# Kernel optimization log

Measured on AMD Instinct MI355X. Metric: run time of the kernel, lower is better.

Reference implementation:

```python
import jax, jax.numpy as jnp
import numpy as np

B, N, A, H, MID = 256, 128, 15, 32, 256  # batch, nodes(=in_channels), actions, EQL-proxy hidden, critic mid_weight


def _glorot(k, shape):
    lim = float(np.sqrt(6.0 / (shape[0] + shape[1])))
    return jax.random.uniform(k, shape, jnp.float32, -lim, lim)


def setup_inputs() -> dict:
    key = jax.random.key(0)
    ks = jax.random.split(key, 10)
    obs = jax.random.normal(ks[0], (B, N), jnp.float32)
    return dict(
        obs=obs,
        # messenger EQL proxy: 4 -> H -> 1
        mw1=_glorot(ks[1], (4, H)), mb1=jnp.zeros((H,), jnp.float32),
        mw2=_glorot(ks[2], (H, 1)), mb2=jnp.zeros((1,), jnp.float32),
        # actor EQL proxy: 3 -> H -> 1
        aw1=_glorot(ks[3], (3, H)), ab1=jnp.zeros((H,), jnp.float32),
        aw2=_glorot(ks[4], (H, 1)), ab2=jnp.zeros((1,), jnp.float32),
        # critic MLP: N -> MID -> MID -> MID -> 1 (depth=4)
        cw1=_glorot(ks[5], (N, MID)), cb1=jnp.zeros((MID,), jnp.float32),
        cw2=_glorot(ks[6], (MID, MID)), cb2=jnp.zeros((MID,), jnp.float32),
        cw3=_glorot(ks[7], (MID, MID)), cb3=jnp.zeros((MID,), jnp.float32),
        cw4=_glorot(ks[8], (MID, 1)), cb4=jnp.zeros((1,), jnp.float32),
    )


def reference(obs, mw1, mb1, mw2, mb2, aw1, ab1, aw2, ab2,
              cw1, cb1, cw2, cb2, cw3, cb3, cw4, cb4):
    b, n = obs.shape
    coor = jnp.arange(n, dtype=jnp.float32) / n  # append_index coordinate channel
    x = jnp.stack([obs, jnp.broadcast_to(coor, obs.shape)], axis=-1)  # [B,n,2]

    # all-pairs message pass: msg_in[b,i,j] = concat(x[b,i], x[b,j])  -> [B,n,n,4]
    xi = jnp.broadcast_to(x[:, :, None, :], (b, n, n, 2))
    xj = jnp.broadcast_to(x[:, None, :, :], (b, n, n, 2))
    msg_in = jnp.concatenate([xi, xj], axis=-1)
    messages = jax.nn.relu(msg_in @ mw1 + mb1) @ mw2 + mb2  # [B,n,n,1]
    msg = jnp.sum(messages, axis=-2)[..., 0]  # sum over j, squeeze -> [B,n]

    # append_index again on the aggregated messages
    m = jnp.stack([msg, jnp.broadcast_to(coor, msg.shape)], axis=-1)  # [B,n,2]

    # node x action cross: am[b,i,a] = concat(m[b,i], a)  -> [B,n,A,3]
    acts = jnp.arange(A, dtype=jnp.float32)[None, None, :, None]
    mi = jnp.broadcast_to(m[:, :, None, :], (b, n, A, 2))
    aj = jnp.broadcast_to(acts, (b, n, A, 1))
    am = jnp.concatenate([mi, aj], axis=-1)
    am_messages = jax.nn.relu(am @ aw1 + ab1) @ aw2 + ab2  # [B,n,A,1]
    logits = jnp.sum(am_messages, axis=-3)[..., 0]  # sum over nodes (obs_dim=-3) -> [B,A]

    # critic MLP on raw obs
    h = jax.nn.relu(obs @ cw1 + cb1)
    h = jax.nn.relu(h @ cw2 + cb2)
    h = jax.nn.relu(h @ cw3 + cb3)
    value = h @ cw4 + cb4  # [B,1]
    return logits, value
```

## Files before the change

kernel.cpp:

```cpp
#include <hip/hip_runtime.h>

#define BB    256
#define NN    128
#define AA    15
#define HH    32
#define MIDD  256
#define NCRIT 16

typedef _Float16 h2_t  __attribute__((ext_vector_type(2)));
typedef _Float16 f16x8 __attribute__((ext_vector_type(8)));
typedef float    f32x4 __attribute__((ext_vector_type(4)));

struct MsgS {
    _Float16 vh[NN][HH];
    float4   p4[8][NN];
    float    part[4][16][8];
    float    msg[NN];
};
struct CriS {
    _Float16 hA[2][16][264];
};

__global__ __launch_bounds__(512, 4) void gacq_v9(
    const float* __restrict__ obs,
    const float* __restrict__ mw1, const float* __restrict__ mb1,
    const float* __restrict__ mw2, const float* __restrict__ mb2,
    const float* __restrict__ aw1, const float* __restrict__ ab1,
    const float* __restrict__ aw2, const float* __restrict__ ab2,
    const float* __restrict__ cw1, const float* __restrict__ cb1,
    const float* __restrict__ cw2, const float* __restrict__ cb2,
    const float* __restrict__ cw3, const float* __restrict__ cb3,
    const float* __restrict__ cw4, const float* __restrict__ cb4,
    float* __restrict__ out)
{
    __shared__ __align__(16) float aux_s[356];
    __shared__ __align__(16) float obs_s[NN];
    __shared__ __align__(16) union { MsgS m; CriS c; } u_s;

    const int blk  = blockIdx.x;
    const int t    = threadIdx.x;
    const int lane = t & 63;

    if (blk >= NCRIT) {
        const int b = blk - NCRIT;

        if (t < 354) {
            float v;
            if      (t < 128) v = mw1[t];
            else if (t < 224) v = aw1[t - 128];
            else if (t < 256) v = ab1[t - 224];
            else if (t < 288) v = aw2[t - 256];
            else if (t < 320) v = mw2[t - 288];
            else if (t < 352) v = mb1[t - 320];
            else if (t == 352) v = mb2[0];
            else               v = ab2[0];
            aux_s[t] = v;
        }
        if (t < NN) obs_s[t] = obs[b * NN + t];
        __syncthreads();

        for (int e = t; e < NN * HH / 2; e += 512) {
            const int   j  = e >> 4, kp = e & 15;
            const int   k0 = kp * 2;
            const float cj = (float)j * (1.0f / (float)NN);
            const float v0 = obs_s[j] * aux_s[64 + k0]     + cj * aux_s[96 + k0]     + aux_s[320 + k0];
            const float v1 = obs_s[j] * aux_s[64 + k0 + 1] + cj * aux_s[96 + k0 + 1] + aux_s[320 + k0 + 1];
            h2_t p; p[0] = (_Float16)v0; p[1] = (_Float16)v1;
            *(h2_t*)&u_s.m.vh[j][k0] = p;
        }

        const int kg = t & 7;
        const int rg = (t >> 3) & 15;
        const int jg = t >> 7;

        h2_t u2[8][2], w2h[2];
        w2h[0][0] = (_Float16)aux_s[288 + kg * 4 + 0];
        w2h[0][1] = (_Float16)aux_s[288 + kg * 4 + 1];
        w2h[1][0] = (_Float16)aux_s[288 + kg * 4 + 2];
        w2h[1][1] = (_Float16)aux_s[288 + kg * 4 + 3];
#pragma unroll
        for (int rr = 0; rr < 8; ++rr) {
            const int   row = rg * 8 + rr;
            const float ob  = obs_s[row];
            const float cr  = (float)row * (1.0f / (float)NN);
#pragma unroll
            for (int kp = 0; kp < 2; ++kp) {
                const int k0 = kg * 4 + kp * 2;
                u2[rr][kp][0] = (_Float16)(ob * aux_s[k0]     + cr * aux_s[32 + k0]);
                u2[rr][kp][1] = (_Float16)(ob * aux_s[k0 + 1] + cr * aux_s[32 + k0 + 1]);
            }
        }
        __syncthreads();

        float acc[8];
#pragma unroll
        for (int rr = 0; rr < 8; ++rr) acc[rr] = 0.f;
        const int j0 = jg * 32;
        {
            const h2_t   zero  = (h2_t)((_Float16)0);
            const uint2* vbase = (const uint2*)&u_s.m.vh[0][kg * 4];
            uint2 vc = vbase[j0 * 8];
#pragma unroll 4
            for (int jj = 0; jj < 32; ++jj) {
                const int   nj = j0 + ((jj + 1) & 31);
                const uint2 vn = vbase[nj * 8];
                const h2_t  va = __builtin_bit_cast(h2_t, vc.x);
                const h2_t  vb = __builtin_bit_cast(h2_t, vc.y);
#pragma unroll
                for (int rr = 0; rr < 8; ++rr) {
                    h2_t s0 = u2[rr][0] + va;
                    h2_t s1 = u2[rr][1] + vb;
                    s0 = __builtin_elementwise_max(s0, zero);
                    s1 = __builtin_elementwise_max(s1, zero);
                    acc[rr] = __builtin_amdgcn_fdot2(s0, w2h[0], acc[rr], false);
                    acc[rr] = __builtin_amdgcn_fdot2(s1, w2h[1], acc[rr], false);
                }
                vc = vn;
            }
        }
#pragma unroll
        for (int m = 1; m <= 4; m <<= 1)
#pragma unroll
            for (int rr = 0; rr < 8; ++rr) acc[rr] += __shfl_xor(acc[rr], m);
        if (kg == 0) {
            *(float4*)&u_s.m.part[jg][rg][0] = make_float4(acc[0], acc[1], acc[2], acc[3]);
            *(float4*)&u_s.m.part[jg][rg][4] = make_float4(acc[4], acc[5], acc[6], acc[7]);
        }
        __syncthreads();

        if (t < NN) {
            float m = (float)NN * aux_s[352];
#pragma unroll
            for (int g = 0; g < 4; ++g) m += u_s.m.part[g][t >> 3][t & 7];
            u_s.m.msg[t] = m;
        }
        __syncthreads();

#pragma unroll
        for (int it = 0; it < 2; ++it) {
            const int   row = t & 127;
            const int   c   = (t >> 7) + it * 4;
            const float mi  = u_s.m.msg[row];
            const float cr  = (float)row * (1.0f / (float)NN);
            const int   k0  = c * 4;
            float4 p;
            p.x = mi * aux_s[128 + k0 + 0] + cr * aux_s[160 + k0 + 0] + aux_s[224 + k0 + 0];
            p.y = mi * aux_s[128 + k0 + 1] + cr * aux_s[160 + k0 + 1] + aux_s[224 + k0 + 1];
            p.z = mi * aux_s[128 + k0 + 2] + cr * aux_s[160 + k0 + 2] + aux_s[224 + k0 + 2];
            p.w = mi * aux_s[128 + k0 + 3] + cr * aux_s[160 + k0 + 3] + aux_s[224 + k0 + 3];
            u_s.m.p4[c][row] = p;
        }
        __syncthreads();

        {
            const int   a   = t >> 5;
            const int   sub = t & 31;
            const float fa  = (float)a;
            float qa[HH];
#pragma unroll
            for (int k = 0; k < HH; ++k) qa[k] = fa * aux_s[192 + k];
            float s0 = 0.f, s1 = 0.f, s2 = 0.f, s3 = 0.f;
#pragma unroll
            for (int m = 0; m < 4; ++m) {
                const int row = sub + 32 * m;
#pragma unroll
                for (int c = 0; c < 8; ++c) {
                    const float4 p4 = u_s.m.p4[c][row];
                    const float4 w4 = *(const float4*)&aux_s[256 + c * 4];
                    const int    k0 = c * 4;
                    s0 += fmaxf(p4.x + qa[k0 + 0], 0.f) * w4.x;
                    s1 += fmaxf(p4.y + qa[k0 + 1], 0.f) * w4.y;
                    s2 += fmaxf(p4.z + qa[k0 + 2], 0.f) * w4.z;
                    s3 += fmaxf(p4.w + qa[k0 + 3], 0.f) * w4.w;
                }
            }
            float s = (s0 + s1) + (s2 + s3);
#pragma unroll
            for (int off = 1; off < 32; off <<= 1) s += __shfl_xor(s, off);
            if (sub == 0 && a < AA)
                out[b * AA + a] = s + (float)NN * aux_s[353];
        }
    } else {
        const int b0 = blk * 16;

        for (int e = t; e < 16 * NN; e += 512)
            u_s.c.hA[0][e >> 7][e & 127] = (_Float16)obs[(b0 + (e >> 7)) * NN + (e & 127)];
        __syncthreads();

        const int w    = t >> 6;
        const int arow = lane & 15;
        const int koff = (lane >> 4) * 8;
        const int n0   = w * 32;

        auto critLayer = [&](const _Float16 (&Ain)[16][264], _Float16 (&Aout)[16][264],
                             const float* __restrict__ W, const float* __restrict__ bias,
                             const int Kd) {
            f32x4 acc0 = {0.f, 0.f, 0.f, 0.f};
            f32x4 acc1 = {0.f, 0.f, 0.f, 0.f};
            for (int ks = 0; ks < Kd; ks += 32) {
                const f16x8  af = *(const f16x8*)&Ain[arow][ks + koff];
                const float* wp = W + (size_t)(ks + koff) * MIDD + n0 + arow;
                f16x8 bf0, bf1;
#pragma unroll
                for (int j = 0; j < 8; ++j) {
                    bf0[j] = (_Float16)wp[j * MIDD];
                    bf1[j] = (_Float16)wp[j * MIDD + 16];
                }
                acc0 = __builtin_amdgcn_mfma_f32_16x16x32_f16(af, bf0, acc0, 0, 0, 0);
                acc1 = __builtin_amdgcn_mfma_f32_16x16x32_f16(af, bf1, acc1, 0, 0, 0);
            }
            const float b0v = bias[n0 + arow];
            const float b1v = bias[n0 + 16 + arow];
#pragma unroll
            for (int reg = 0; reg < 4; ++reg) {
                const int i = (lane >> 4) * 4 + reg;
                Aout[i][n0 + arow]      = (_Float16)fmaxf(acc0[reg] + b0v, 0.f);
                Aout[i][n0 + 16 + arow] = (_Float16)fmaxf(acc1[reg] + b1v, 0.f);
            }
        };

        critLayer(u_s.c.hA[0], u_s.c.hA[1], cw1, cb1, 128);
        __syncthreads();
        critLayer(u_s.c.hA[1], u_s.c.hA[0], cw2, cb2, 256);
        __syncthreads();
        critLayer(u_s.c.hA[0], u_s.c.hA[1], cw3, cb3, 256);
        __syncthreads();

        {
            const int i  = t >> 5;
            const int sl = t & 31;
            float s = 0.f;
#pragma unroll
            for (int j = 0; j < 8; ++j)
                s += (float)u_s.c.hA[1][i][sl * 8 + j] * cw4[sl * 8 + j];
#pragma unroll
            for (int off = 1; off < 32; off <<= 1) s += __shfl_xor(s, off);
            if (sl == 0) out[BB * AA + b0 + i] = s + cb4[0];
        }
    }
}

extern "C" void kernel_launch(void* const* d_in, const int* in_sizes, int n_in,
                              void* d_out, int out_size, void* d_ws, size_t ws_size,
                              hipStream_t stream) {
    const float* obs = (const float*)d_in[0];
    const float* mw1 = (const float*)d_in[1];
    const float* mb1 = (const float*)d_in[2];
    const float* mw2 = (const float*)d_in[3];
    const float* mb2 = (const float*)d_in[4];
    const float* aw1 = (const float*)d_in[5];
    const float* ab1 = (const float*)d_in[6];
    const float* aw2 = (const float*)d_in[7];
    const float* ab2 = (const float*)d_in[8];
    const float* cw1 = (const float*)d_in[9];
    const float* cb1 = (const float*)d_in[10];
    const float* cw2 = (const float*)d_in[11];
    const float* cb2 = (const float*)d_in[12];
    const float* cw3 = (const float*)d_in[13];
    const float* cb3 = (const float*)d_in[14];
    const float* cw4 = (const float*)d_in[15];
    const float* cb4 = (const float*)d_in[16];
    float* out = (float*)d_out;

    gacq_v9<<<dim3(BB + NCRIT), dim3(512), 0, stream>>>(
        obs, mw1, mb1, mw2, mb2, aw1, ab1, aw2, ab2,
        cw1, cb1, cw2, cb2, cw3, cb3, cw4, cb4, out);
}
```

Measured before the change: 17.16 us.

## Double block size to 1024 threads, halving per-thread work in all phases

Launches 1024 threads per block instead of 512 and re-splits every phase across them. The message loop now covers 16 j-columns per thread group instead of 32, and the 8 partial sums are reduced straight into the actor projection, which removes one barrier and the msg buffer. Each critic wave computes one 16-column MFMA tile instead of two. This buys more latency hiding and shorter per-thread serial chains, at the cost of heavier register pressure under launch_bounds(1024,4), fewer blocks resident per CU, and more redundant weight reads for the critic.

```diff
diff --git a/kernel.cpp b/kernel.cpp
--- a/kernel.cpp
+++ b/kernel.cpp
@@ -14,14 +14,13 @@
 struct MsgS {
     _Float16 vh[NN][HH];
     float4   p4[8][NN];
-    float    part[4][16][8];
-    float    msg[NN];
+    float    part[8][16][8];
 };
 struct CriS {
     _Float16 hA[2][16][264];
 };
 
-__global__ __launch_bounds__(512, 4) void gacq_v9(
+__global__ __launch_bounds__(1024, 4) void gacq_v10(
     const float* __restrict__ obs,
     const float* __restrict__ mw1, const float* __restrict__ mb1,
     const float* __restrict__ mw2, const float* __restrict__ mb2,
@@ -56,10 +55,12 @@
             else               v = ab2[0];
             aux_s[t] = v;
         }
-        if (t < NN) obs_s[t] = obs[b * NN + t];
-        __syncthreads();
-
-        for (int e = t; e < NN * HH / 2; e += 512) {
+        if (t >= 512 && t < 512 + NN) obs_s[t - 512] = obs[b * NN + (t - 512)];
+        __syncthreads();
+
+#pragma unroll
+        for (int it = 0; it < 2; ++it) {
+            const int   e  = t + it * 1024;
             const int   j  = e >> 4, kp = e & 15;
             const int   k0 = kp * 2;
             const float cj = (float)j * (1.0f / (float)NN);
@@ -95,14 +96,14 @@
         float acc[8];
 #pragma unroll
         for (int rr = 0; rr < 8; ++rr) acc[rr] = 0.f;
-        const int j0 = jg * 32;
+        const int j0 = jg * 16;
         {
             const h2_t   zero  = (h2_t)((_Float16)0);
             const uint2* vbase = (const uint2*)&u_s.m.vh[0][kg * 4];
             uint2 vc = vbase[j0 * 8];
 #pragma unroll 4
-            for (int jj = 0; jj < 32; ++jj) {
-                const int   nj = j0 + ((jj + 1) & 31);
+            for (int jj = 0; jj < 16; ++jj) {
+                const int   nj = j0 + ((jj + 1) & 15);
                 const uint2 vn = vbase[nj * 8];
                 const h2_t  va = __builtin_bit_cast(h2_t, vc.x);
                 const h2_t  vb = __builtin_bit_cast(h2_t, vc.y);
@@ -128,21 +129,14 @@
         }
         __syncthreads();
 
-        if (t < NN) {
-            float m = (float)NN * aux_s[352];
-#pragma unroll
-            for (int g = 0; g < 4; ++g) m += u_s.m.part[g][t >> 3][t & 7];
-            u_s.m.msg[t] = m;
-        }
-        __syncthreads();
-
-#pragma unroll
-        for (int it = 0; it < 2; ++it) {
-            const int   row = t & 127;
-            const int   c   = (t >> 7) + it * 4;
-            const float mi  = u_s.m.msg[row];
-            const float cr  = (float)row * (1.0f / (float)NN);
-            const int   k0  = c * 4;
+        {
+            const int row = t & 127;
+            const int c   = t >> 7;
+            float mi = (float)NN * aux_s[352];
+#pragma unroll
+            for (int g = 0; g < 8; ++g) mi += u_s.m.part[g][row >> 3][row & 7];
+            const float cr = (float)row * (1.0f / (float)NN);
+            const int   k0 = c * 4;
             float4 p;
             p.x = mi * aux_s[128 + k0 + 0] + cr * aux_s[160 + k0 + 0] + aux_s[224 + k0 + 0];
             p.y = mi * aux_s[128 + k0 + 1] + cr * aux_s[160 + k0 + 1] + aux_s[224 + k0 + 1];
@@ -153,16 +147,16 @@
         __syncthreads();
 
         {
-            const int   a   = t >> 5;
-            const int   sub = t & 31;
+            const int   a   = t >> 6;
+            const int   sub = lane;
             const float fa  = (float)a;
             float qa[HH];
 #pragma unroll
             for (int k = 0; k < HH; ++k) qa[k] = fa * aux_s[192 + k];
             float s0 = 0.f, s1 = 0.f, s2 = 0.f, s3 = 0.f;
 #pragma unroll
-            for (int m = 0; m < 4; ++m) {
-                const int row = sub + 32 * m;
+            for (int m = 0; m < 2; ++m) {
+                const int row = sub + 64 * m;
 #pragma unroll
                 for (int c = 0; c < 8; ++c) {
                     const float4 p4 = u_s.m.p4[c][row];
@@ -176,46 +170,42 @@
             }
             float s = (s0 + s1) + (s2 + s3);
 #pragma unroll
-            for (int off = 1; off < 32; off <<= 1) s += __shfl_xor(s, off);
+            for (int off = 1; off < 64; off <<= 1) s += __shfl_xor(s, off);
             if (sub == 0 && a < AA)
                 out[b * AA + a] = s + (float)NN * aux_s[353];
         }
     } else {
         const int b0 = blk * 16;
 
-        for (int e = t; e < 16 * NN; e += 512)
+#pragma unroll
+        for (int it = 0; it < 2; ++it) {
+            const int e = t + it * 1024;
             u_s.c.hA[0][e >> 7][e & 127] = (_Float16)obs[(b0 + (e >> 7)) * NN + (e & 127)];
+        }
         __syncthreads();
 
         const int w    = t >> 6;
         const int arow = lane & 15;
         const int koff = (lane >> 4) * 8;
-        const int n0   = w * 32;
+        const int n0   = w * 16;
 
         auto critLayer = [&](const _Float16 (&Ain)[16][264], _Float16 (&Aout)[16][264],
                              const float* __restrict__ W, const float* __restrict__ bias,
                              const int Kd) {
-            f32x4 acc0 = {0.f, 0.f, 0.f, 0.f};
-            f32x4 acc1 = {0.f, 0.f, 0.f, 0.f};
+            f32x4 acc = {0.f, 0.f, 0.f, 0.f};
             for (int ks = 0; ks < Kd; ks += 32) {
                 const f16x8  af = *(const f16x8*)&Ain[arow][ks + koff];
                 const float* wp = W + (size_t)(ks + koff) * MIDD + n0 + arow;
-                f16x8 bf0, bf1;
-#pragma unroll
-                for (int j = 0; j < 8; ++j) {
-                    bf0[j] = (_Float16)wp[j * MIDD];
-                    bf1[j] = (_Float16)wp[j * MIDD + 16];
-                }
-                acc0 = __builtin_amdgcn_mfma_f32_16x16x32_f16(af, bf0, acc0, 0, 0, 0);
-                acc1 = __builtin_amdgcn_mfma_f32_16x16x32_f16(af, bf1, acc1, 0, 0, 0);
-            }
-            const float b0v = bias[n0 + arow];
-            const float b1v = bias[n0 + 16 + arow];
+                f16x8 bf;
+#pragma unroll
+                for (int j = 0; j < 8; ++j) bf[j] = (_Float16)wp[j * MIDD];
+                acc = __builtin_amdgcn_mfma_f32_16x16x32_f16(af, bf, acc, 0, 0, 0);
+            }
+            const float bv = bias[n0 + arow];
 #pragma unroll
             for (int reg = 0; reg < 4; ++reg) {
                 const int i = (lane >> 4) * 4 + reg;
-                Aout[i][n0 + arow]      = (_Float16)fmaxf(acc0[reg] + b0v, 0.f);
-                Aout[i][n0 + 16 + arow] = (_Float16)fmaxf(acc1[reg] + b1v, 0.f);
+                Aout[i][n0 + arow] = (_Float16)fmaxf(acc[reg] + bv, 0.f);
             }
         };
 
@@ -227,15 +217,14 @@
         __syncthreads();
 
         {
-            const int i  = t >> 5;
-            const int sl = t & 31;
+            const int i = t >> 6;
             float s = 0.f;
 #pragma unroll
-            for (int j = 0; j < 8; ++j)
-                s += (float)u_s.c.hA[1][i][sl * 8 + j] * cw4[sl * 8 + j];
-#pragma unroll
-            for (int off = 1; off < 32; off <<= 1) s += __shfl_xor(s, off);
-            if (sl == 0) out[BB * AA + b0 + i] = s + cb4[0];
+            for (int j = 0; j < 4; ++j)
+                s += (float)u_s.c.hA[1][i][lane * 4 + j] * cw4[lane * 4 + j];
+#pragma unroll
+            for (int off = 1; off < 64; off <<= 1) s += __shfl_xor(s, off);
+            if (lane == 0) out[BB * AA + b0 + i] = s + cb4[0];
         }
     }
 }
@@ -262,7 +251,7 @@
     const float* cb4 = (const float*)d_in[16];
     float* out = (float*)d_out;
 
-    gacq_v9<<<dim3(BB + NCRIT), dim3(512), 0, stream>>>(
+    gacq_v10<<<dim3(BB + NCRIT), dim3(1024), 0, stream>>>(
         obs, mw1, mb1, mw2, mb2, aw1, ab1, aw2, ab2,
         cw1, cb1, cw2, cb2, cw3, cb3, cw4, cb4, out);
 }
```

New measurement: 21.96 us. 1.28x slower.

## Keep message-pass operands in registers, one wave per 16-row tile

Applied to the files above, without the earlier changes.

Each wave now owns 16 rows and splits the 128 j columns across 8 lane groups. Every thread computes its own 16 j-side fp16 hidden values in registers, so the shared-memory vh table and its barrier go away. The reduction is done entirely with wave shuffles, which removes the part/msg shared buffers and two __syncthreads. The cost is more register pressure (u2, v2 and acc at 16 each), redundant computation of the j-side values across waves, and a longer shuffle reduction chain.

```diff
diff --git a/kernel.cpp b/kernel.cpp
--- a/kernel.cpp
+++ b/kernel.cpp
@@ -11,17 +11,10 @@
 typedef _Float16 f16x8 __attribute__((ext_vector_type(8)));
 typedef float    f32x4 __attribute__((ext_vector_type(4)));
 
-struct MsgS {
-    _Float16 vh[NN][HH];
-    float4   p4[8][NN];
-    float    part[4][16][8];
-    float    msg[NN];
-};
-struct CriS {
-    _Float16 hA[2][16][264];
-};
-
-__global__ __launch_bounds__(512, 4) void gacq_v9(
+struct MsgS { float4   p4[8][NN]; };
+struct CriS { _Float16 hA[2][16][264]; };
+
+__global__ __launch_bounds__(512, 4) void gacq_v11(
     const float* __restrict__ obs,
     const float* __restrict__ mw1, const float* __restrict__ mb1,
     const float* __restrict__ mw2, const float* __restrict__ mb2,
@@ -40,6 +33,7 @@
     const int blk  = blockIdx.x;
     const int t    = threadIdx.x;
     const int lane = t & 63;
+    const int w    = t >> 6;
 
     if (blk >= NCRIT) {
         const int b = blk - NCRIT;
@@ -59,28 +53,19 @@
         if (t < NN) obs_s[t] = obs[b * NN + t];
         __syncthreads();
 
-        for (int e = t; e < NN * HH / 2; e += 512) {
-            const int   j  = e >> 4, kp = e & 15;
-            const int   k0 = kp * 2;
-            const float cj = (float)j * (1.0f / (float)NN);
-            const float v0 = obs_s[j] * aux_s[64 + k0]     + cj * aux_s[96 + k0]     + aux_s[320 + k0];
-            const float v1 = obs_s[j] * aux_s[64 + k0 + 1] + cj * aux_s[96 + k0 + 1] + aux_s[320 + k0 + 1];
-            h2_t p; p[0] = (_Float16)v0; p[1] = (_Float16)v1;
-            *(h2_t*)&u_s.m.vh[j][k0] = p;
-        }
-
-        const int kg = t & 7;
-        const int rg = (t >> 3) & 15;
-        const int jg = t >> 7;
-
-        h2_t u2[8][2], w2h[2];
+        const int kg = lane & 7;
+        const int jg = (lane >> 3) & 7;
+
+        h2_t w2h[2];
         w2h[0][0] = (_Float16)aux_s[288 + kg * 4 + 0];
         w2h[0][1] = (_Float16)aux_s[288 + kg * 4 + 1];
         w2h[1][0] = (_Float16)aux_s[288 + kg * 4 + 2];
         w2h[1][1] = (_Float16)aux_s[288 + kg * 4 + 3];
-#pragma unroll
-        for (int rr = 0; rr < 8; ++rr) {
-            const int   row = rg * 8 + rr;
+
+        h2_t u2[16][2];
+#pragma unroll
+        for (int rr = 0; rr < 16; ++rr) {
+            const int   row = w * 16 + rr;
             const float ob  = obs_s[row];
             const float cr  = (float)row * (1.0f / (float)NN);
 #pragma unroll
@@ -90,24 +75,31 @@
                 u2[rr][kp][1] = (_Float16)(ob * aux_s[k0 + 1] + cr * aux_s[32 + k0 + 1]);
             }
         }
-        __syncthreads();
-
-        float acc[8];
-#pragma unroll
-        for (int rr = 0; rr < 8; ++rr) acc[rr] = 0.f;
-        const int j0 = jg * 32;
-        {
-            const h2_t   zero  = (h2_t)((_Float16)0);
-            const uint2* vbase = (const uint2*)&u_s.m.vh[0][kg * 4];
-            uint2 vc = vbase[j0 * 8];
-#pragma unroll 4
-            for (int jj = 0; jj < 32; ++jj) {
-                const int   nj = j0 + ((jj + 1) & 31);
-                const uint2 vn = vbase[nj * 8];
-                const h2_t  va = __builtin_bit_cast(h2_t, vc.x);
-                const h2_t  vb = __builtin_bit_cast(h2_t, vc.y);
-#pragma unroll
-                for (int rr = 0; rr < 8; ++rr) {
+        h2_t v2[16][2];
+#pragma unroll
+        for (int jj = 0; jj < 16; ++jj) {
+            const int   j  = jg * 16 + jj;
+            const float ob = obs_s[j];
+            const float cj = (float)j * (1.0f / (float)NN);
+#pragma unroll
+            for (int kp = 0; kp < 2; ++kp) {
+                const int k0 = kg * 4 + kp * 2;
+                v2[jj][kp][0] = (_Float16)(ob * aux_s[64 + k0]     + cj * aux_s[96 + k0]     + aux_s[320 + k0]);
+                v2[jj][kp][1] = (_Float16)(ob * aux_s[64 + k0 + 1] + cj * aux_s[96 + k0 + 1] + aux_s[320 + k0 + 1]);
+            }
+        }
+
+        float acc[16];
+#pragma unroll
+        for (int rr = 0; rr < 16; ++rr) acc[rr] = 0.f;
+        {
+            const h2_t zero = (h2_t)((_Float16)0);
+#pragma unroll
+            for (int jj = 0; jj < 16; ++jj) {
+                const h2_t va = v2[jj][0];
+                const h2_t vb = v2[jj][1];
+#pragma unroll
+                for (int rr = 0; rr < 16; ++rr) {
                     h2_t s0 = u2[rr][0] + va;
                     h2_t s1 = u2[rr][1] + vb;
                     s0 = __builtin_elementwise_max(s0, zero);
@@ -115,40 +107,32 @@
                     acc[rr] = __builtin_amdgcn_fdot2(s0, w2h[0], acc[rr], false);
                     acc[rr] = __builtin_amdgcn_fdot2(s1, w2h[1], acc[rr], false);
                 }
-                vc = vn;
-            }
-        }
-#pragma unroll
-        for (int m = 1; m <= 4; m <<= 1)
-#pragma unroll
-            for (int rr = 0; rr < 8; ++rr) acc[rr] += __shfl_xor(acc[rr], m);
-        if (kg == 0) {
-            *(float4*)&u_s.m.part[jg][rg][0] = make_float4(acc[0], acc[1], acc[2], acc[3]);
-            *(float4*)&u_s.m.part[jg][rg][4] = make_float4(acc[4], acc[5], acc[6], acc[7]);
-        }
-        __syncthreads();
-
-        if (t < NN) {
-            float m = (float)NN * aux_s[352];
-#pragma unroll
-            for (int g = 0; g < 4; ++g) m += u_s.m.part[g][t >> 3][t & 7];
-            u_s.m.msg[t] = m;
-        }
-        __syncthreads();
-
-#pragma unroll
-        for (int it = 0; it < 2; ++it) {
-            const int   row = t & 127;
-            const int   c   = (t >> 7) + it * 4;
-            const float mi  = u_s.m.msg[row];
+            }
+        }
+#pragma unroll
+        for (int m = 1; m <= 32; m <<= 1)
+#pragma unroll
+            for (int rr = 0; rr < 16; ++rr) acc[rr] += __shfl_xor(acc[rr], m);
+
+        {
+            const int rrL = lane & 15;
+            float mi = acc[0];
+#pragma unroll
+            for (int r2 = 1; r2 < 16; ++r2) mi = (rrL == r2) ? acc[r2] : mi;
+            mi += (float)NN * aux_s[352];
+            const int   row = w * 16 + rrL;
             const float cr  = (float)row * (1.0f / (float)NN);
-            const int   k0  = c * 4;
-            float4 p;
-            p.x = mi * aux_s[128 + k0 + 0] + cr * aux_s[160 + k0 + 0] + aux_s[224 + k0 + 0];
-            p.y = mi * aux_s[128 + k0 + 1] + cr * aux_s[160 + k0 + 1] + aux_s[224 + k0 + 1];
-            p.z = mi * aux_s[128 + k0 + 2] + cr * aux_s[160 + k0 + 2] + aux_s[224 + k0 + 2];
-            p.w = mi * aux_s[128 + k0 + 3] + cr * aux_s[160 + k0 + 3] + aux_s[224 + k0 + 3];
-            u_s.m.p4[c][row] = p;
+#pragma unroll
+            for (int cc = 0; cc < 2; ++cc) {
+                const int c  = (lane >> 4) + cc * 4;
+                const int k0 = c * 4;
+                float4 p;
+                p.x = mi * aux_s[128 + k0 + 0] + cr * aux_s[160 + k0 + 0] + aux_s[224 + k0 + 0];
+                p.y = mi * aux_s[128 + k0 + 1] + cr * aux_s[160 + k0 + 1] + aux_s[224 + k0 + 1];
+                p.z = mi * aux_s[128 + k0 + 2] + cr * aux_s[160 + k0 + 2] + aux_s[224 + k0 + 2];
+                p.w = mi * aux_s[128 + k0 + 3] + cr * aux_s[160 + k0 + 3] + aux_s[224 + k0 + 3];
+                u_s.m.p4[c][row] = p;
+            }
         }
         __syncthreads();
 
@@ -187,7 +171,6 @@
             u_s.c.hA[0][e >> 7][e & 127] = (_Float16)obs[(b0 + (e >> 7)) * NN + (e & 127)];
         __syncthreads();
 
-        const int w    = t >> 6;
         const int arow = lane & 15;
         const int koff = (lane >> 4) * 8;
         const int n0   = w * 32;
@@ -262,7 +245,7 @@
     const float* cb4 = (const float*)d_in[16];
     float* out = (float*)d_out;
 
-    gacq_v9<<<dim3(BB + NCRIT), dim3(512), 0, stream>>>(
+    gacq_v11<<<dim3(BB + NCRIT), dim3(512), 0, stream>>>(
         obs, mw1, mb1, mw2, mb2, aw1, ab1, aw2, ab2,
         cw1, cb1, cw2, cb2, cw3, cb3, cw4, cb4, out);
 }
```

New measurement: 18.60 us. 8.4% more time.

## Split critic into second kernel fed by fp16 weights pre-converted in first

Applied to the files above, without the earlier changes.

The single fused kernel is split in two. The first kernel runs the message/actor blocks plus 16 extra blocks that convert the critic weights cw1–cw3 from fp32 to fp16 into workspace. A second kernel then runs the critic MLP, reading half-width fp16 weights instead of converting fp32 loads on the fly. The aim is to cut critic global-load bytes and conversion work, at the cost of a second launch, a serial dependency between the kernels, and a workspace round trip. It also folds the msg shared array into registers, removing one barrier.

```diff
diff --git a/kernel.cpp b/kernel.cpp
--- a/kernel.cpp
+++ b/kernel.cpp
@@ -5,7 +5,13 @@
 #define AA    15
 #define HH    32
 #define MIDD  256
+#define NCVT  16
 #define NCRIT 16
+
+#define W1E   32768
+#define W2OFF 32768
+#define W3OFF 98304
+#define WTOT  163840
 
 typedef _Float16 h2_t  __attribute__((ext_vector_type(2)));
 typedef _Float16 f16x8 __attribute__((ext_vector_type(8)));
@@ -15,228 +21,243 @@
     _Float16 vh[NN][HH];
     float4   p4[8][NN];
     float    part[4][16][8];
-    float    msg[NN];
 };
-struct CriS {
-    _Float16 hA[2][16][264];
-};
-
-__global__ __launch_bounds__(512, 4) void gacq_v9(
+
+__global__ __launch_bounds__(512, 4) void gacq_msg(
     const float* __restrict__ obs,
     const float* __restrict__ mw1, const float* __restrict__ mb1,
     const float* __restrict__ mw2, const float* __restrict__ mb2,
     const float* __restrict__ aw1, const float* __restrict__ ab1,
     const float* __restrict__ aw2, const float* __restrict__ ab2,
-    const float* __restrict__ cw1, const float* __restrict__ cb1,
-    const float* __restrict__ cw2, const float* __restrict__ cb2,
-    const float* __restrict__ cw3, const float* __restrict__ cb3,
-    const float* __restrict__ cw4, const float* __restrict__ cb4,
-    float* __restrict__ out)
+    const float* __restrict__ cw1, const float* __restrict__ cw2,
+    const float* __restrict__ cw3,
+    float* __restrict__ out, _Float16* __restrict__ ws16)
 {
     __shared__ __align__(16) float aux_s[356];
     __shared__ __align__(16) float obs_s[NN];
-    __shared__ __align__(16) union { MsgS m; CriS c; } u_s;
-
-    const int blk  = blockIdx.x;
-    const int t    = threadIdx.x;
-    const int lane = t & 63;
-
-    if (blk >= NCRIT) {
-        const int b = blk - NCRIT;
-
-        if (t < 354) {
-            float v;
-            if      (t < 128) v = mw1[t];
-            else if (t < 224) v = aw1[t - 128];
-            else if (t < 256) v = ab1[t - 224];
-            else if (t < 288) v = aw2[t - 256];
-            else if (t < 320) v = mw2[t - 288];
-            else if (t < 352) v = mb1[t - 320];
-            else if (t == 352) v = mb2[0];
-            else               v = ab2[0];
-            aux_s[t] = v;
-        }
-        if (t < NN) obs_s[t] = obs[b * NN + t];
-        __syncthreads();
-
-        for (int e = t; e < NN * HH / 2; e += 512) {
-            const int   j  = e >> 4, kp = e & 15;
-            const int   k0 = kp * 2;
-            const float cj = (float)j * (1.0f / (float)NN);
-            const float v0 = obs_s[j] * aux_s[64 + k0]     + cj * aux_s[96 + k0]     + aux_s[320 + k0];
-            const float v1 = obs_s[j] * aux_s[64 + k0 + 1] + cj * aux_s[96 + k0 + 1] + aux_s[320 + k0 + 1];
-            h2_t p; p[0] = (_Float16)v0; p[1] = (_Float16)v1;
-            *(h2_t*)&u_s.m.vh[j][k0] = p;
-        }
-
-        const int kg = t & 7;
-        const int rg = (t >> 3) & 15;
-        const int jg = t >> 7;
-
-        h2_t u2[8][2], w2h[2];
-        w2h[0][0] = (_Float16)aux_s[288 + kg * 4 + 0];
-        w2h[0][1] = (_Float16)aux_s[288 + kg * 4 + 1];
-        w2h[1][0] = (_Float16)aux_s[288 + kg * 4 + 2];
-        w2h[1][1] = (_Float16)aux_s[288 + kg * 4 + 3];
-#pragma unroll
-        for (int rr = 0; rr < 8; ++rr) {
-            const int   row = rg * 8 + rr;
-            const float ob  = obs_s[row];
-            const float cr  = (float)row * (1.0f / (float)NN);
-#pragma unroll
-            for (int kp = 0; kp < 2; ++kp) {
-                const int k0 = kg * 4 + kp * 2;
-                u2[rr][kp][0] = (_Float16)(ob * aux_s[k0]     + cr * aux_s[32 + k0]);
-                u2[rr][kp][1] = (_Float16)(ob * aux_s[k0 + 1] + cr * aux_s[32 + k0 + 1]);
+    __shared__ __align__(16) MsgS m_s;
+
+    const int blk = blockIdx.x;
+    const int t   = threadIdx.x;
+
+    if (blk >= BB) {
+        const int cb   = blk - BB;
+        const int base = cb * (WTOT / NCVT);
+#pragma unroll 4
+        for (int i = 0; i < (WTOT / NCVT) / 512; ++i) {
+            const int idx = base + i * 512 + t;
+            float src;
+            if      (idx < W2OFF) src = cw1[idx];
+            else if (idx < W3OFF) src = cw2[idx - W2OFF];
+            else                  src = cw3[idx - W3OFF];
+            ws16[idx] = (_Float16)src;
+        }
+        return;
+    }
+
+    const int b = blk;
+
+    if (t < 354) {
+        float v;
+        if      (t < 128) v = mw1[t];
+        else if (t < 224) v = aw1[t - 128];
+        else if (t < 256) v = ab1[t - 224];
+        else if (t < 288) v = aw2[t - 256];
+        else if (t < 320) v = mw2[t - 288];
+        else if (t < 352) v = mb1[t - 320];
+        else if (t == 352) v = mb2[0];
+        else               v = ab2[0];
+        aux_s[t] = v;
+    }
+    if (t < NN) obs_s[t] = obs[b * NN + t];
+    __syncthreads();
+
+    for (int e = t; e < NN * HH / 2; e += 512) {
+        const int   j  = e >> 4, kp = e & 15;
+        const int   k0 = kp * 2;
+        const float cj = (float)j * (1.0f / (float)NN);
+        const float v0 = obs_s[j] * aux_s[64 + k0]     + cj * aux_s[96 + k0]     + aux_s[320 + k0];
+        const float v1 = obs_s[j] * aux_s[64 + k0 + 1] + cj * aux_s[96 + k0 + 1] + aux_s[320 + k0 + 1];
+        h2_t p; p[0] = (_Float16)v0; p[1] = (_Float16)v1;
+        *(h2_t*)&m_s.vh[j][k0] = p;
+    }
+
+    const int kg = t & 7;
+    const int rg = (t >> 3) & 15;
+    const int jg = t >> 7;
+
+    h2_t u2[8][2], w2h[2];
+    w2h[0][0] = (_Float16)aux_s[288 + kg * 4 + 0];
+    w2h[0][1] = (_Float16)aux_s[288 + kg * 4 + 1];
+    w2h[1][0] = (_Float16)aux_s[288 + kg * 4 + 2];
+    w2h[1][1] = (_Float16)aux_s[288 + kg * 4 + 3];
+#pragma unroll
+    for (int rr = 0; rr < 8; ++rr) {
+        const int   row = rg * 8 + rr;
+        const float ob  = obs_s[row];
+        const float cr  = (float)row * (1.0f / (float)NN);
+#pragma unroll
+        for (int kp = 0; kp < 2; ++kp) {
+            const int k0 = kg * 4 + kp * 2;
+            u2[rr][kp][0] = (_Float16)(ob * aux_s[k0]     + cr * aux_s[32 + k0]);
+            u2[rr][kp][1] = (_Float16)(ob * aux_s[k0 + 1] + cr * aux_s[32 + k0 + 1]);
+        }
+    }
+    __syncthreads();
+
+    float acc[8];
+#pragma unroll
+    for (int rr = 0; rr < 8; ++rr) acc[rr] = 0.f;
+    const int j0 = jg * 32;
+    {
+        const h2_t   zero  = (h2_t)((_Float16)0);
+        const uint2* vbase = (const uint2*)&m_s.vh[0][kg * 4];
+        uint2 vc = vbase[j0 * 8];
+#pragma unroll 4
+        for (int jj = 0; jj < 32; ++jj) {
+            const int   nj = j0 + ((jj + 1) & 31);
+            const uint2 vn = vbase[nj * 8];
+            const h2_t  va = __builtin_bit_cast(h2_t, vc.x);
+            const h2_t  vb = __builtin_bit_cast(h2_t, vc.y);
+#pragma unroll
+            for (int rr = 0; rr < 8; ++rr) {
+                h2_t s0 = u2[rr][0] + va;
+                h2_t s1 = u2[rr][1] + vb;
+                s0 = __builtin_elementwise_max(s0, zero);
+                s1 = __builtin_elementwise_max(s1, zero);
+                acc[rr] = __builtin_amdgcn_fdot2(s0, w2h[0], acc[rr], false);
+                acc[rr] = __builtin_amdgcn_fdot2(s1, w2h[1], acc[rr], false);
             }
-        }
-        __syncthreads();
-
-        float acc[8];
-#pragma unroll
-        for (int rr = 0; rr < 8; ++rr) acc[rr] = 0.f;
-        const int j0 = jg * 32;
-        {
-            const h2_t   zero  = (h2_t)((_Float16)0);
-            const uint2* vbase = (const uint2*)&u_s.m.vh[0][kg * 4];
-            uint2 vc = vbase[j0 * 8];
-#pragma unroll 4
-            for (int jj = 0; jj < 32; ++jj) {
-                const int   nj = j0 + ((jj + 1) & 31);
-                const uint2 vn = vbase[nj * 8];
-                const h2_t  va = __builtin_bit_cast(h2_t, vc.x);
-                const h2_t  vb = __builtin_bit_cast(h2_t, vc.y);
-#pragma unroll
-                for (int rr = 0; rr < 8; ++rr) {
-                    h2_t s0 = u2[rr][0] + va;
-                    h2_t s1 = u2[rr][1] + vb;
-                    s0 = __builtin_elementwise_max(s0, zero);
-                    s1 = __builtin_elementwise_max(s1, zero);
-                    acc[rr] = __builtin_amdgcn_fdot2(s0, w2h[0], acc[rr], false);
-                    acc[rr] = __builtin_amdgcn_fdot2(s1, w2h[1], acc[rr], false);
-                }
-                vc = vn;
-            }
-        }
-#pragma unroll
-        for (int m = 1; m <= 4; m <<= 1)
-#pragma unroll
-            for (int rr = 0; rr < 8; ++rr) acc[rr] += __shfl_xor(acc[rr], m);
-        if (kg == 0) {
-            *(float4*)&u_s.m.part[jg][rg][0] = make_float4(acc[0], acc[1], acc[2], acc[3]);
-            *(float4*)&u_s.m.part[jg][rg][4] = make_float4(acc[4], acc[5], acc[6], acc[7]);
-        }
-        __syncthreads();
-
-        if (t < NN) {
-            float m = (float)NN * aux_s[352];
-#pragma unroll
-            for (int g = 0; g < 4; ++g) m += u_s.m.part[g][t >> 3][t & 7];
-            u_s.m.msg[t] = m;
-        }
-        __syncthreads();
-
+            vc = vn;
+        }
+    }
+#pragma unroll
+    for (int m = 1; m <= 4; m <<= 1)
+#pragma unroll
+        for (int rr = 0; rr < 8; ++rr) acc[rr] += __shfl_xor(acc[rr], m);
+    if (kg == 0) {
+        *(float4*)&m_s.part[jg][rg][0] = make_float4(acc[0], acc[1], acc[2], acc[3]);
+        *(float4*)&m_s.part[jg][rg][4] = make_float4(acc[4], acc[5], acc[6], acc[7]);
+    }
+    __syncthreads();
+
+    {
+        const int row = t & 127;
+        float mi = (float)NN * aux_s[352];
+#pragma unroll
+        for (int g = 0; g < 4; ++g) mi += m_s.part[g][row >> 3][row & 7];
+        const float cr = (float)row * (1.0f / (float)NN);
 #pragma unroll
         for (int it = 0; it < 2; ++it) {
-            const int   row = t & 127;
-            const int   c   = (t >> 7) + it * 4;
-            const float mi  = u_s.m.msg[row];
-            const float cr  = (float)row * (1.0f / (float)NN);
-            const int   k0  = c * 4;
+            const int c  = (t >> 7) + it * 4;
+            const int k0 = c * 4;
             float4 p;
             p.x = mi * aux_s[128 + k0 + 0] + cr * aux_s[160 + k0 + 0] + aux_s[224 + k0 + 0];
             p.y = mi * aux_s[128 + k0 + 1] + cr * aux_s[160 + k0 + 1] + aux_s[224 + k0 + 1];
             p.z = mi * aux_s[128 + k0 + 2] + cr * aux_s[160 + k0 + 2] + aux_s[224 + k0 + 2];
             p.w = mi * aux_s[128 + k0 + 3] + cr * aux_s[160 + k0 + 3] + aux_s[224 + k0 + 3];
-            u_s.m.p4[c][row] = p;
-        }
-        __syncthreads();
-
-        {
-            const int   a   = t >> 5;
-            const int   sub = t & 31;
-            const float fa  = (float)a;
-            float qa[HH];
-#pragma unroll
-            for (int k = 0; k < HH; ++k) qa[k] = fa * aux_s[192 + k];
-            float s0 = 0.f, s1 = 0.f, s2 = 0.f, s3 = 0.f;
-#pragma unroll
-            for (int m = 0; m < 4; ++m) {
-                const int row = sub + 32 * m;
-#pragma unroll
-                for (int c = 0; c < 8; ++c) {
-                    const float4 p4 = u_s.m.p4[c][row];
-                    const float4 w4 = *(const float4*)&aux_s[256 + c * 4];
-                    const int    k0 = c * 4;
-                    s0 += fmaxf(p4.x + qa[k0 + 0], 0.f) * w4.x;
-                    s1 += fmaxf(p4.y + qa[k0 + 1], 0.f) * w4.y;
-                    s2 += fmaxf(p4.z + qa[k0 + 2], 0.f) * w4.z;
-                    s3 += fmaxf(p4.w + qa[k0 + 3], 0.f) * w4.w;
-                }
+            m_s.p4[c][row] = p;
+        }
+    }
+    __syncthreads();
+
+    {
+        const int   a   = t >> 5;
+        const int   sub = t & 31;
+        const float fa  = (float)a;
+        float qa[HH];
+#pragma unroll
+        for (int k = 0; k < HH; ++k) qa[k] = fa * aux_s[192 + k];
+        float s0 = 0.f, s1 = 0.f, s2 = 0.f, s3 = 0.f;
+#pragma unroll
+        for (int m = 0; m < 4; ++m) {
+            const int row = sub + 32 * m;
+#pragma unroll
+            for (int c = 0; c < 8; ++c) {
+                const float4 p4 = m_s.p4[c][row];
+                const float4 w4 = *(const float4*)&aux_s[256 + c * 4];
+                const int    k0 = c * 4;
+                s0 += fmaxf(p4.x + qa[k0 + 0], 0.f) * w4.x;
+                s1 += fmaxf(p4.y + qa[k0 + 1], 0.f) * w4.y;
+                s2 += fmaxf(p4.z + qa[k0 + 2], 0.f) * w4.z;
+                s3 += fmaxf(p4.w + qa[k0 + 3], 0.f) * w4.w;
             }
-            float s = (s0 + s1) + (s2 + s3);
-#pragma unroll
-            for (int off = 1; off < 32; off <<= 1) s += __shfl_xor(s, off);
-            if (sub == 0 && a < AA)
-                out[b * AA + a] = s + (float)NN * aux_s[353];
-        }
-    } else {
-        const int b0 = blk * 16;
-
-        for (int e = t; e < 16 * NN; e += 512)
-            u_s.c.hA[0][e >> 7][e & 127] = (_Float16)obs[(b0 + (e >> 7)) * NN + (e & 127)];
-        __syncthreads();
-
-        const int w    = t >> 6;
-        const int arow = lane & 15;
-        const int koff = (lane >> 4) * 8;
-        const int n0   = w * 32;
-
-        auto critLayer = [&](const _Float16 (&Ain)[16][264], _Float16 (&Aout)[16][264],
-                             const float* __restrict__ W, const float* __restrict__ bias,
-                             const int Kd) {
-            f32x4 acc0 = {0.f, 0.f, 0.f, 0.f};
-            f32x4 acc1 = {0.f, 0.f, 0.f, 0.f};
-            for (int ks = 0; ks < Kd; ks += 32) {
-                const f16x8  af = *(const f16x8*)&Ain[arow][ks + koff];
-                const float* wp = W + (size_t)(ks + koff) * MIDD + n0 + arow;
-                f16x8 bf0, bf1;
-#pragma unroll
-                for (int j = 0; j < 8; ++j) {
-                    bf0[j] = (_Float16)wp[j * MIDD];
-                    bf1[j] = (_Float16)wp[j * MIDD + 16];
-                }
-                acc0 = __builtin_amdgcn_mfma_f32_16x16x32_f16(af, bf0, acc0, 0, 0, 0);
-                acc1 = __builtin_amdgcn_mfma_f32_16x16x32_f16(af, bf1, acc1, 0, 0, 0);
+        }
+        float s = (s0 + s1) + (s2 + s3);
+#pragma unroll
+        for (int off = 1; off < 32; off <<= 1) s += __shfl_xor(s, off);
+        if (sub == 0 && a < AA)
+            out[b * AA + a] = s + (float)NN * aux_s[353];
+    }
+}
+
+__global__ __launch_bounds__(512, 4) void gacq_crit(
+    const float* __restrict__ obs, const _Float16* __restrict__ ws16,
+    const float* __restrict__ cb1, const float* __restrict__ cb2,
+    const float* __restrict__ cb3,
+    const float* __restrict__ cw4, const float* __restrict__ cb4,
+    float* __restrict__ out)
+{
+    __shared__ __align__(16) _Float16 hA[2][16][264];
+
+    const int blk  = blockIdx.x;
+    const int t    = threadIdx.x;
+    const int lane = t & 63;
+    const int w    = t >> 6;
+    const int b0   = blk * 16;
+
+    for (int e = t; e < 16 * NN; e += 512)
+        hA[0][e >> 7][e & 127] = (_Float16)obs[(b0 + (e >> 7)) * NN + (e & 127)];
+    __syncthreads();
+
+    const int arow = lane & 15;
+    const int koff = (lane >> 4) * 8;
+    const int n0   = w * 32;
+
+    auto critLayer = [&](const _Float16 (&Ain)[16][264], _Float16 (&Aout)[16][264],
+                         const _Float16* __restrict__ W16, const float* __restrict__ bias,
+                         const int Kd) {
+        f32x4 acc0 = {0.f, 0.f, 0.f, 0.f};
+        f32x4 acc1 = {0.f, 0.f, 0.f, 0.f};
+        for (int ks = 0; ks < Kd; ks += 32) {
+            const f16x8     af = *(const f16x8*)&Ain[arow][ks + koff];
+            const _Float16* wp = W16 + (size_t)(ks + koff) * MIDD + n0 + arow;
+            f16x8 bf0, bf1;
+#pragma unroll
+            for (int j = 0; j < 8; ++j) {
+                bf0[j] = wp[j * MIDD];
+                bf1[j] = wp[j * MIDD + 16];
             }
-            const float b0v = bias[n0 + arow];
-            const float b1v = bias[n0 + 16 + arow];
-#pragma unroll
-            for (int reg = 0; reg < 4; ++reg) {
-                const int i = (lane >> 4) * 4 + reg;
-                Aout[i][n0 + arow]      = (_Float16)fmaxf(acc0[reg] + b0v, 0.f);
-                Aout[i][n0 + 16 + arow] = (_Float16)fmaxf(acc1[reg] + b1v, 0.f);
-            }
-        };
-
-        critLayer(u_s.c.hA[0], u_s.c.hA[1], cw1, cb1, 128);
-        __syncthreads();
-        critLayer(u_s.c.hA[1], u_s.c.hA[0], cw2, cb2, 256);
-        __syncthreads();
-        critLayer(u_s.c.hA[0], u_s.c.hA[1], cw3, cb3, 256);
-        __syncthreads();
-
-        {
-            const int i  = t >> 5;
-            const int sl = t & 31;
-            float s = 0.f;
-#pragma unroll
-            for (int j = 0; j < 8; ++j)
-                s += (float)u_s.c.hA[1][i][sl * 8 + j] * cw4[sl * 8 + j];
-#pragma unroll
-            for (int off = 1; off < 32; off <<= 1) s += __shfl_xor(s, off);
-            if (sl == 0) out[BB * AA + b0 + i] = s + cb4[0];
-        }
+            acc0 = __builtin_amdgcn_mfma_f32_16x16x32_f16(af, bf0, acc0, 0, 0, 0);
+            acc1 = __builtin_amdgcn_mfma_f32_16x16x32_f16(af, bf1, acc1, 0, 0, 0);
+        }
+        const float b0v = bias[n0 + arow];
+        const float b1v = bias[n0 + 16 + arow];
+#pragma unroll
+        for (int reg = 0; reg < 4; ++reg) {
+            const int i = (lane >> 4) * 4 + reg;
+            Aout[i][n0 + arow]      = (_Float16)fmaxf(acc0[reg] + b0v, 0.f);
+            Aout[i][n0 + 16 + arow] = (_Float16)fmaxf(acc1[reg] + b1v, 0.f);
+        }
+    };
+
+    critLayer(hA[0], hA[1], ws16,         cb1, 128);
+    __syncthreads();
+    critLayer(hA[1], hA[0], ws16 + W2OFF, cb2, 256);
+    __syncthreads();
+    critLayer(hA[0], hA[1], ws16 + W3OFF, cb3, 256);
+    __syncthreads();
+
+    {
+        const int i  = t >> 5;
+        const int sl = t & 31;
+        float s = 0.f;
+#pragma unroll
+        for (int j = 0; j < 8; ++j)
+            s += (float)hA[1][i][sl * 8 + j] * cw4[sl * 8 + j];
+#pragma unroll
+        for (int off = 1; off < 32; off <<= 1) s += __shfl_xor(s, off);
+        if (sl == 0) out[BB * AA + b0 + i] = s + cb4[0];
     }
 }
 
@@ -260,9 +281,13 @@
     const float* cb3 = (const float*)d_in[14];
     const float* cw4 = (const float*)d_in[15];
     const float* cb4 = (const float*)d_in[16];
-    float* out = (float*)d_out;
-
-    gacq_v9<<<dim3(BB + NCRIT), dim3(512), 0, stream>>>(
+    float*     out  = (float*)d_out;
+    _Float16*  ws16 = (_Float16*)d_ws;
+
+    gacq_msg<<<dim3(BB + NCVT), dim3(512), 0, stream>>>(
         obs, mw1, mb1, mw2, mb2, aw1, ab1, aw2, ab2,
-        cw1, cb1, cw2, cb2, cw3, cb3, cw4, cb4, out);
+        cw1, cw2, cw3, out, ws16);
+
+    gacq_crit<<<dim3(NCRIT), dim3(512), 0, stream>>>(
+        obs, ws16, cb1, cb2, cb3, cw4, cb4, out);
 }
```

Result: slower. 25.19 us (+46.8%).
